# Performance work log

Hardware: AMD Instinct MI355X
Metric: run time of the kernel (lower is better)

The kernel has to match this reference:

```python
import jax, jax.numpy as jnp
import numpy as np

B = 32768
Z_DIM = 64
X_DIM = 256
HIDDEN = 512
T = 8            # num_transforms
NBINS = 8
TAIL = 25.0
MULT = 3 * NBINS - 1   # widths + heights + interior derivatives = 23
MIN_W = 1e-3
MIN_H = 1e-3
MIN_D = 1e-3


def _masks():
    # MADE degrees (nflows, random_mask=False)
    d_in = np.arange(1, Z_DIM + 1)                      # input degrees 1..D
    h = np.arange(HIDDEN) % (Z_DIM - 1) + 1             # hidden degrees
    o = np.arange(Z_DIM * MULT) // MULT + 1             # output degrees, MULT contiguous per feature
    m1 = (h[:, None] >= d_in[None, :]).astype(np.float32)   # [H, D]
    m2 = (h[:, None] >= h[None, :]).astype(np.float32)      # [H, H]
    m3 = (o[:, None] > h[None, :]).astype(np.float32)       # [D*MULT, H] strict for output layer
    return jnp.asarray(m1), jnp.asarray(m2), jnp.asarray(m3)


def _rq_spline_fwd(z, uw, uh, ud):
    """Unconstrained rational-quadratic spline with linear tails (forward).
    z: [B, D]; uw/uh: [B, D, NBINS]; ud: [B, D, NBINS-1].
    Returns (outputs [B,D], logabsdet [B,D])."""
    const = np.log(np.exp(1.0 - MIN_D) - 1.0)
    pad = jnp.full(ud.shape[:-1] + (1,), const, ud.dtype)
    ud = jnp.concatenate([pad, ud, pad], axis=-1)       # [B, D, NBINS+1]

    widths = jax.nn.softmax(uw, axis=-1)
    widths = MIN_W + (1.0 - MIN_W * NBINS) * widths
    zero = jnp.zeros(widths.shape[:-1] + (1,), widths.dtype)
    cumw = jnp.concatenate([zero, jnp.cumsum(widths, axis=-1)], axis=-1)
    cumw = -TAIL + 2.0 * TAIL * cumw
    cumw = cumw.at[..., 0].set(-TAIL).at[..., -1].set(TAIL)
    widths = cumw[..., 1:] - cumw[..., :-1]

    derivs = MIN_D + jax.nn.softplus(ud)

    heights = jax.nn.softmax(uh, axis=-1)
    heights = MIN_H + (1.0 - MIN_H * NBINS) * heights
    cumh = jnp.concatenate([zero, jnp.cumsum(heights, axis=-1)], axis=-1)
    cumh = -TAIL + 2.0 * TAIL * cumh
    cumh = cumh.at[..., 0].set(-TAIL).at[..., -1].set(TAIL)
    heights = cumh[..., 1:] - cumh[..., :-1]

    delta = heights / widths

    z_in = jnp.clip(z, -TAIL, TAIL)
    edges = cumw.at[..., -1].add(1e-6)                  # nflows searchsorted eps
    idx = jnp.sum(z_in[..., None] >= edges, axis=-1) - 1
    idx = jnp.clip(idx, 0, NBINS - 1)

    g = lambda a: jnp.take_along_axis(a, idx[..., None], axis=-1)[..., 0]
    in_cw = g(cumw); in_w = g(widths)
    in_ch = g(cumh); in_h = g(heights)
    in_dl = g(delta)
    d0 = g(derivs); d1 = g(derivs[..., 1:])

    th = (z_in - in_cw) / in_w
    th1 = th * (1.0 - th)
    num = in_h * (in_dl * th * th + d0 * th1)
    den = in_dl + (d0 + d1 - 2.0 * in_dl) * th1
    out = in_ch + num / den
    dnum = in_dl ** 2 * (d1 * th * th + 2.0 * in_dl * th1 + d0 * (1.0 - th) ** 2)
    lad = jnp.log(dnum) - 2.0 * jnp.log(den)

    inside = (z >= -TAIL) & (z <= TAIL)
    return jnp.where(inside, out, z), jnp.where(inside, lad, 0.0)


def setup_inputs() -> dict:
    key = jax.random.key(0)
    ks = jax.random.split(key, 10)
    s = 0.05  # small init scale keeps spline params in a sane regime
    return {
        "z": jax.random.normal(ks[0], (B, Z_DIM), jnp.float32),
        "x": jax.random.normal(ks[1], (B, X_DIM), jnp.float32),
        "W1": jax.random.normal(ks[2], (T, HIDDEN, Z_DIM), jnp.float32) * s,
        "b1": jax.random.normal(ks[3], (T, HIDDEN), jnp.float32) * s,
        "Wc": jax.random.normal(ks[4], (T, HIDDEN, X_DIM), jnp.float32) * s,
        "bc": jax.random.normal(ks[5], (T, HIDDEN), jnp.float32) * s,
        "W2": jax.random.normal(ks[6], (T, HIDDEN, HIDDEN), jnp.float32) * s,
        "b2": jax.random.normal(ks[7], (T, HIDDEN), jnp.float32) * s,
        "W3": jax.random.normal(ks[8], (T, Z_DIM * MULT, HIDDEN), jnp.float32) * s,
        "b3": jax.random.normal(ks[9], (T, Z_DIM * MULT), jnp.float32) * s,
    }


def reference(z, x, W1, b1, Wc, bc, W2, b2, W3, b3):
    """log q(z|x) of the composed MADE-RQ-spline flow, shape [B]."""
    m1, m2, m3 = _masks()
    inv_sqrt_h = 1.0 / np.sqrt(HIDDEN)
    cur = z
    total_lad = jnp.zeros(z.shape[0], z.dtype)
    for t in range(T):
        # MADE: masked initial layer + context layer, one masked feedforward block (linear->relu), masked output layer
        h = cur @ (W1[t] * m1).T + b1[t] + x @ Wc[t].T + bc[t]
        h = jax.nn.relu(h @ (W2[t] * m2).T + b2[t])
        p = (h @ (W3[t] * m3).T + b3[t]).reshape(-1, Z_DIM, MULT)
        uw = p[..., :NBINS] * inv_sqrt_h
        uh = p[..., NBINS:2 * NBINS] * inv_sqrt_h
        ud = p[..., 2 * NBINS:]
        cur, lad = _rq_spline_fwd(cur, uw, uh, ud)
        total_lad = total_lad + lad.sum(axis=-1)
    log_base = -0.5 * jnp.sum(cur ** 2, axis=-1) - 0.5 * Z_DIM * np.log(2.0 * np.pi)
    return log_base + total_lad
```

## Files before the change

kernel.cpp:

```cpp
#include <hip/hip_runtime.h>
#include <cstdint>
#include <cstddef>

#define B_ROWS 32768
#define ZD 64
#define XD 256
#define HID 512
#define T_STEPS 8
#define MULT 23
#define MPAD 24
#define NOUT 1472
#define NPAD 1536
#define K1 320
#define PSTRIDE 200

typedef float f32x4 __attribute__((ext_vector_type(4)));
typedef short s16x8 __attribute__((ext_vector_type(8)));

__device__ __forceinline__ unsigned short f2bf(float f) {
  unsigned int u = __float_as_uint(f);
  u = (u + 0x7FFFu + ((u >> 16) & 1u)) >> 16;
  return (unsigned short)u;
}
__device__ __forceinline__ float bf2f(unsigned short s) {
  return __uint_as_float(((unsigned int)s) << 16);
}

__device__ __forceinline__ int permP(int n) {
  return (n < 72) ? (n / 9) + 63 * (n % 9)
                  : ((n - 72) >> 3) + 8 + 63 * ((n - 72) & 7);
}
__device__ __forceinline__ int degP(int n) {
  return (n < 72) ? (n / 9) + 1 : ((n - 72) >> 3) + 9;
}


__global__ void prep_weights(const float* __restrict__ W1, const float* __restrict__ Wc,
                             const float* __restrict__ W2, const float* __restrict__ W3,
                             const float* __restrict__ b1, const float* __restrict__ bc,
                             const float* __restrict__ b2, const float* __restrict__ b3,
                             unsigned short* __restrict__ w1c, unsigned short* __restrict__ w2c,
                             unsigned short* __restrict__ w3c,
                             float* __restrict__ ob1, float* __restrict__ ob2,
                             float* __restrict__ ob3) {
  const int S1 = T_STEPS * HID * K1;
  const int S2 = S1 + T_STEPS * HID * HID;
  const int S3 = S2 + T_STEPS * NPAD * HID;
  const int S4 = S3 + T_STEPS * HID;
  const int S5 = S4 + T_STEPS * HID;
  const int S6 = S5 + T_STEPS * NPAD;
  int i = blockIdx.x * 256 + threadIdx.x;
  if (i < S1) {
    int t = i / (HID * K1);
    int r = i - t * (HID * K1);
    int n = r / K1;
    int k = r - n * K1;
    int on = permP(n);
    float v;
    if (k < ZD) v = ((on % 63) >= k) ? W1[((size_t)t * HID + on) * ZD + k] : 0.0f;
    else        v = Wc[((size_t)t * HID + on) * XD + (k - ZD)];
    w1c[i] = f2bf(v);
  } else if (i < S2) {
    int j = i - S1;
    int t = j / (HID * HID);
    int r = j - t * (HID * HID);
    int n = r / HID;
    int k = r - n * HID;
    float v = 0.0f;
    if (degP(n) >= degP(k))
      v = W2[((size_t)t * HID + permP(n)) * HID + permP(k)];
    w2c[j] = f2bf(v);
  } else if (i < S3) {
    int j = i - S2;
    int t = j / (NPAD * HID);
    int r = j - t * (NPAD * HID);
    int n = r / HID;
    int k = r - n * HID;
    int d = n / MPAD;
    int jj = n - d * MPAD;
    float v = 0.0f;
    if (jj < MULT && d >= degP(k))
      v = W3[((size_t)t * NOUT + d * MULT + jj) * HID + permP(k)];
    w3c[j] = f2bf(v);
  } else if (i < S4) {
    int j = i - S3;
    int t = j / HID, n = j - t * HID;
    int on = permP(n);
    ob1[j] = b1[(size_t)t * HID + on] + bc[(size_t)t * HID + on];
  } else if (i < S5) {
    int j = i - S4;
    int t = j / HID, n = j - t * HID;
    ob2[j] = b2[(size_t)t * HID + permP(n)];
  } else if (i < S6) {
    int j = i - S5;
    int t = j / NPAD;
    int n = j - t * NPAD;
    int d = n / MPAD;
    int jj = n - d * MPAD;
    ob3[j] = (jj < MULT) ? b3[(size_t)t * NOUT + d * MULT + jj] : 0.0f;
  }
}

__global__ void prep_data(const float* __restrict__ x, const float* __restrict__ z,
                          unsigned short* __restrict__ A1,
                          float* __restrict__ curf, float* __restrict__ out) {
  const int SX = B_ROWS * XD;
  int i = blockIdx.x * 256 + threadIdx.x;
  if (i < SX) {
    int b = i >> 8;
    int j = i & 255;
    A1[(size_t)b * K1 + ZD + j] = f2bf(x[i]);
  } else {
    int j = i - SX;
    if (j < B_ROWS * ZD) {
      int b = j >> 6;
      int d = j & 63;
      float zv = z[j];
      A1[(size_t)b * K1 + d] = f2bf(zv);
      curf[j] = zv;
      if (d == 0) out[b] = -58.81206612509905f;
    }
  }
}


#define ASYNC16(gp, lp) __builtin_amdgcn_global_load_lds( \
    (__attribute__((address_space(1))) unsigned int*)(gp), \
    (__attribute__((address_space(3))) unsigned int*)(lp), 16, 0, 0)

#define WAITV(n) asm volatile("s_waitcnt vmcnt(" #n ")" ::: "memory")


__global__ __launch_bounds__(256, 3) void gemm_bias(
    const unsigned short* __restrict__ A,
    const unsigned short* __restrict__ Bw,
    const float* __restrict__ bias,
    unsigned short* __restrict__ C,
    int M, int N, int K, int relu, int tri)
{
  __shared__ alignas(16) unsigned short lS[3][8192];

  const int tid  = threadIdx.x;
  const int lane = tid & 63;
  const int wave = tid >> 6;

  const int lin = blockIdx.y * 4 + blockIdx.x;
  const int xcd = lin & 7;
  const int loc = lin >> 3;
  const int m0 = (xcd * 32 + (loc >> 2)) * 128;
  const int n0 = (loc & 3) * 128;
  const int Keff = tri ? min(K, 192 + n0) : K;
  const int nIter = Keff >> 5;

  const int wm = (wave >> 1) * 64;
  const int wn = (wave & 1) * 64;

  const int f    = tid * 16;
  const int row0 = f >> 6;
  const int colb = f & 63;

  char* gA0 = (char*)A  + ((size_t)(m0 + row0) * K) * 2 + colb;
  char* gA1 = gA0 + (size_t)64 * K * 2;
  char* gB0 = (char*)Bw + ((size_t)(n0 + row0) * K) * 2 + colb;
  char* gB1 = gB0 + (size_t)64 * K * 2;

  f32x4 acc[4][4];
#pragma unroll
  for (int i = 0; i < 4; i++)
#pragma unroll
    for (int j = 0; j < 4; j++) acc[i][j] = (f32x4){0.f, 0.f, 0.f, 0.f};

  const int fr = lane & 15;
  const int fk = (lane >> 4) * 8;

#define STAGEB(sp) do { \
    unsigned short* s_ = (sp) + wave * 512; \
    ASYNC16(gA0, s_); \
    ASYNC16(gA1, s_ + 2048); \
    ASYNC16(gB0, s_ + 4096); \
    ASYNC16(gB1, s_ + 6144); \
    gA0 += 64; gA1 += 64; gB0 += 64; gB1 += 64; \
  } while (0)

  STAGEB(lS[0]);
  STAGEB(lS[1]);

  for (int k = 0; k < nIter; ++k) {
    __builtin_amdgcn_sched_barrier(0);
    if (k + 2 < nIter) STAGEB(lS[0] + ((k + 2) % 3) * 8192);
    const int nv = nIter - 1 - k;
    if (nv >= 2)      WAITV(8);
    else if (nv == 1) WAITV(4);
    else              WAITV(0);
    __builtin_amdgcn_s_barrier();
    __builtin_amdgcn_sched_barrier(0);

    const unsigned short* cs = lS[0] + (k % 3) * 8192;
    s16x8 a[4], b[4];
#pragma unroll
    for (int i = 0; i < 4; i++)
      a[i] = *(const s16x8*)(cs + (wm + i * 16 + fr) * 32 + fk);
#pragma unroll
    for (int j = 0; j < 4; j++)
      b[j] = *(const s16x8*)(cs + 4096 + (wn + j * 16 + fr) * 32 + fk);

#pragma unroll
    for (int i = 0; i < 4; i++)
#pragma unroll
      for (int j = 0; j < 4; j++)
        acc[i][j] = __builtin_amdgcn_mfma_f32_16x16x32_bf16(a[i], b[j], acc[i][j], 0, 0, 0);

    __builtin_amdgcn_sched_barrier(0);
    __builtin_amdgcn_s_barrier();
  }
#undef STAGEB

#pragma unroll
  for (int j = 0; j < 4; j++) {
    const int col = n0 + wn + j * 16 + fr;
    const float bv = bias[col];
#pragma unroll
    for (int i = 0; i < 4; i++) {
      const int rbase = m0 + wm + i * 16 + (lane >> 4) * 4;
#pragma unroll
      for (int r = 0; r < 4; r++) {
        float v = acc[i][j][r] + bv;
        if (relu) v = fmaxf(v, 0.0f);
        C[(size_t)(rbase + r) * N + col] = f2bf(v);
      }
    }
  }
}


__device__ __forceinline__ void rq_spline(const unsigned short* __restrict__ pp,
                                          float zv, float& zn, float& lad) {
  const float TAILC = 25.0f;
  const float MIN_WC = 0.001f;
  const float MIN_DC = 0.001f;
  const float SCALE2 = 0.06376007120095582f;
  const float LN2 = 0.6931471805599453f;

  s16x8 vw = *(const s16x8*)(pp);
  s16x8 vh = *(const s16x8*)(pp + 8);
  s16x8 vd = *(const s16x8*)(pp + 16);

  bool inside = (zv >= -TAILC) && (zv <= TAILC);
  float z_in = fminf(fmaxf(zv, -TAILC), TAILC);

  float ew[8], eh[8], sw = 0.f, sh = 0.f;
#pragma unroll
  for (int i = 0; i < 8; i++) {
    ew[i] = exp2f(bf2f((unsigned short)vw[i]) * SCALE2); sw += ew[i];
  }
#pragma unroll
  for (int i = 0; i < 8; i++) {
    eh[i] = exp2f(bf2f((unsigned short)vh[i]) * SCALE2); sh += eh[i];
  }
  float iw = (1.0f - 8.0f * MIN_WC) / sw;
  float ih = (1.0f - 8.0f * MIN_WC) / sh;

  float cumw[9], cumh[9];
  cumw[0] = -TAILC; cumh[0] = -TAILC;
  float cw = 0.f, ch = 0.f;
#pragma unroll
  for (int i = 0; i < 8; i++) {
    cw += MIN_WC + ew[i] * iw;
    ch += MIN_WC + eh[i] * ih;
    cumw[i + 1] = fmaf(2.0f * TAILC, cw, -TAILC);
    cumh[i + 1] = fmaf(2.0f * TAILC, ch, -TAILC);
  }
  cumw[8] = TAILC; cumh[8] = TAILC;

  int idx = 0;
#pragma unroll
  for (int i = 1; i < 8; i++) idx += (z_in >= cumw[i]) ? 1 : 0;

  float in_cw = 0.f, cw1 = 1.f, in_ch = 0.f, ch1 = 1.f, u0 = 0.f, u1 = 0.f;
#pragma unroll
  for (int i = 0; i < 8; i++) {
    if (i == idx) {
      in_cw = cumw[i]; cw1 = cumw[i + 1];
      in_ch = cumh[i]; ch1 = cumh[i + 1];
      u0 = (i > 0) ? bf2f((unsigned short)vd[i - 1]) : 0.0f;
      u1 = (i < 7) ? bf2f((unsigned short)vd[i]) : 0.0f;
    }
  }
  float dd0 = (idx == 0) ? 1.0f
            : MIN_DC + fmaxf(u0, 0.f) + __logf(1.0f + __expf(-fabsf(u0)));
  float dd1 = (idx == 7) ? 1.0f
            : MIN_DC + fmaxf(u1, 0.f) + __logf(1.0f + __expf(-fabsf(u1)));
  float in_w = cw1 - in_cw;
  float in_h = ch1 - in_ch;

  float delta = in_h / in_w;
  float th  = (z_in - in_cw) / in_w;
  float th1 = th * (1.0f - th);
  float th2 = th * th;
  float num = in_h * (delta * th2 + dd0 * th1);
  float den = delta + (dd0 + dd1 - 2.0f * delta) * th1;
  float outz = in_ch + num / den;
  float omt = 1.0f - th;
  float dnum = delta * delta * (dd1 * th2 + 2.0f * delta * th1 + dd0 * omt * omt);
  float l = LN2 * (__log2f(dnum) - 2.0f * __log2f(den));

  zn  = inside ? outz : zv;
  lad = inside ? l : 0.0f;
}


__global__ __launch_bounds__(256, 2) void gemm3_spline(
    const unsigned short* __restrict__ A,
    const unsigned short* __restrict__ Bw,
    const float* __restrict__ bias,
    float* __restrict__ curf,
    unsigned short* __restrict__ A1,
    float* __restrict__ out,
    int last)
{
  __shared__ alignas(16) union {
    unsigned short stage[3][10240];
    unsigned short p[128 * PSTRIDE];
  } sm;

  const int tid  = threadIdx.x;
  const int lane = tid & 63;
  const int wave = tid >> 6;

  const int lin = blockIdx.y * 8 + blockIdx.x;
  const int xcd = lin & 7;
  const int loc = lin >> 3;
  const int m0 = (xcd * 32 + (loc >> 3)) * 128;
  const int bn = loc & 7;
  const int n0 = bn * 192;
  const int nIter = 2 * (bn + 1);

  const int wm = (wave >> 1) * 64;
  const int wn = (wave & 1) * 96;
  const int fr = lane & 15;
  const int fk = (lane >> 4) * 8;

  const int srow = tid & 127;
  const int sb = m0 + srow;
  const int dl0 = (tid >> 7) * 4;
  const int d0 = bn * 8 + dl0;
  float4 cz = *(const float4*)(curf + (size_t)sb * ZD + d0);
  float bv[6];
#pragma unroll
  for (int j = 0; j < 6; j++) bv[j] = bias[n0 + wn + j * 16 + fr];

  const int f    = tid * 16;
  const int row0 = f >> 6;
  const int colb = f & 63;
  const int K = HID;

  char* gA0 = (char*)A  + ((size_t)(m0 + row0) * K) * 2 + colb;
  char* gA1 = gA0 + (size_t)64 * K * 2;
  char* gB0 = (char*)Bw + ((size_t)(n0 + row0) * K) * 2 + colb;
  char* gB1 = gB0 + (size_t)64 * K * 2;
  char* gB2 = gB1 + (size_t)64 * K * 2;

  f32x4 acc[4][6];
#pragma unroll
  for (int i = 0; i < 4; i++)
#pragma unroll
    for (int j = 0; j < 6; j++) acc[i][j] = (f32x4){0.f, 0.f, 0.f, 0.f};

#define STAGE3(sp) do { \
    unsigned short* s_ = (sp) + wave * 512; \
    ASYNC16(gA0, s_); \
    ASYNC16(gA1, s_ + 2048); \
    ASYNC16(gB0, s_ + 4096); \
    ASYNC16(gB1, s_ + 6144); \
    ASYNC16(gB2, s_ + 8192); \
    gA0 += 64; gA1 += 64; gB0 += 64; gB1 += 64; gB2 += 64; \
  } while (0)

  STAGE3(sm.stage[0]);
  STAGE3(sm.stage[1]);

  for (int k = 0; k < nIter; ++k) {
    __builtin_amdgcn_sched_barrier(0);
    if (k + 2 < nIter) STAGE3(sm.stage[0] + ((k + 2) % 3) * 10240);
    const int nv = nIter - 1 - k;
    if (nv >= 2)      WAITV(10);
    else if (nv == 1) WAITV(5);
    else              WAITV(0);
    __builtin_amdgcn_s_barrier();
    __builtin_amdgcn_sched_barrier(0);

    const unsigned short* cs = sm.stage[0] + (k % 3) * 10240;
    s16x8 a[4], b[6];
#pragma unroll
    for (int i = 0; i < 4; i++)
      a[i] = *(const s16x8*)(cs + (wm + i * 16 + fr) * 32 + fk);
#pragma unroll
    for (int j = 0; j < 6; j++)
      b[j] = *(const s16x8*)(cs + 4096 + (wn + j * 16 + fr) * 32 + fk);

#pragma unroll
    for (int i = 0; i < 4; i++)
#pragma unroll
      for (int j = 0; j < 6; j++)
        acc[i][j] = __builtin_amdgcn_mfma_f32_16x16x32_bf16(a[i], b[j], acc[i][j], 0, 0, 0);

    __builtin_amdgcn_sched_barrier(0);
    __builtin_amdgcn_s_barrier();
  }
#undef STAGE3

#pragma unroll
  for (int j = 0; j < 6; j++) {
    const int col = wn + j * 16 + fr;
#pragma unroll
    for (int i = 0; i < 4; i++) {
      const int rbase = wm + i * 16 + (lane >> 4) * 4;
#pragma unroll
      for (int r = 0; r < 4; r++)
        sm.p[(rbase + r) * PSTRIDE + col] = f2bf(acc[i][j][r] + bv[j]);
    }
  }
  __syncthreads();

  const unsigned short* pp = sm.p + srow * PSTRIDE + dl0 * MPAD;
  float zn0, zn1, zn2, zn3, l0, l1, l2, l3;
  rq_spline(pp,            cz.x, zn0, l0);
  rq_spline(pp + MPAD,     cz.y, zn1, l1);
  rq_spline(pp + 2 * MPAD, cz.z, zn2, l2);
  rq_spline(pp + 3 * MPAD, cz.w, zn3, l3);

  *(float4*)(curf + (size_t)sb * ZD + d0) = make_float4(zn0, zn1, zn2, zn3);
  union { unsigned int u[2]; unsigned short s[4]; } pk;
  pk.s[0] = f2bf(zn0); pk.s[1] = f2bf(zn1); pk.s[2] = f2bf(zn2); pk.s[3] = f2bf(zn3);
  *(uint2*)(A1 + (size_t)sb * K1 + d0) = make_uint2(pk.u[0], pk.u[1]);

  float contrib = l0 + l1 + l2 + l3;
  if (last)
    contrib -= 0.5f * (zn0 * zn0 + zn1 * zn1 + zn2 * zn2 + zn3 * zn3);
  atomicAdd(&out[sb], contrib);
}


extern "C" void kernel_launch(void* const* d_in, const int* in_sizes, int n_in,
                              void* d_out, int out_size, void* d_ws, size_t ws_size,
                              hipStream_t stream)
{
  const float* z  = (const float*)d_in[0];
  const float* x  = (const float*)d_in[1];
  const float* W1 = (const float*)d_in[2];
  const float* b1 = (const float*)d_in[3];
  const float* Wc = (const float*)d_in[4];
  const float* bc = (const float*)d_in[5];
  const float* W2 = (const float*)d_in[6];
  const float* b2 = (const float*)d_in[7];
  const float* W3 = (const float*)d_in[8];
  const float* b3 = (const float*)d_in[9];
  float* out = (float*)d_out;
  char* ws = (char*)d_ws;

  size_t oA1 = 0;
  size_t oH1 = oA1 + (size_t)B_ROWS * K1 * 2;
  size_t oH2 = oH1 + (size_t)B_ROWS * HID * 2;
  size_t oCU = oH2 + (size_t)B_ROWS * HID * 2;
  size_t oW1 = oCU + (size_t)B_ROWS * ZD * 4;
  size_t oW2 = oW1 + (size_t)T_STEPS * HID * K1 * 2;
  size_t oW3 = oW2 + (size_t)T_STEPS * HID * HID * 2;
  size_t oB1 = oW3 + (size_t)T_STEPS * NPAD * HID * 2;
  size_t oB2 = oB1 + (size_t)T_STEPS * HID * 4;
  size_t oB3 = oB2 + (size_t)T_STEPS * HID * 4;

  unsigned short* A1  = (unsigned short*)(ws + oA1);
  unsigned short* h1  = (unsigned short*)(ws + oH1);
  unsigned short* h2  = (unsigned short*)(ws + oH2);
  float* curf = (float*)(ws + oCU);
  unsigned short* w1c = (unsigned short*)(ws + oW1);
  unsigned short* w2c = (unsigned short*)(ws + oW2);
  unsigned short* w3c = (unsigned short*)(ws + oW3);
  float* b1c = (float*)(ws + oB1);
  float* b2p = (float*)(ws + oB2);
  float* b3c = (float*)(ws + oB3);

  const int prepw_total = T_STEPS * (HID * K1 + HID * HID + NPAD * HID + 2 * HID + NPAD);
  prep_weights<<<(prepw_total + 255) / 256, 256, 0, stream>>>(
      W1, Wc, W2, W3, b1, bc, b2, b3, w1c, w2c, w3c, b1c, b2p, b3c);
  const int prepd_total = B_ROWS * (XD + ZD);
  prep_data<<<(prepd_total + 255) / 256, 256, 0, stream>>>(x, z, A1, curf, out);

  for (int t = 0; t < T_STEPS; ++t) {
    gemm_bias<<<dim3(4, B_ROWS / 128), 256, 0, stream>>>(
        A1, w1c + (size_t)t * HID * K1, b1c + (size_t)t * HID, h1,
        B_ROWS, HID, K1, 0, 0);
    gemm_bias<<<dim3(4, B_ROWS / 128), 256, 0, stream>>>(
        h1, w2c + (size_t)t * HID * HID, b2p + (size_t)t * HID, h2,
        B_ROWS, HID, HID, 1, 1);
    gemm3_spline<<<dim3(8, B_ROWS / 128), 256, 0, stream>>>(
        h2, w3c + (size_t)t * NPAD * HID, b3c + (size_t)t * NPAD,
        curf, A1, out, (t == T_STEPS - 1) ? 1 : 0);
  }
}
```

Before: 1.045 ms.

## Load GEMM3 operands directly from global into registers, dropping LDS staging

The output-layer GEMM in the fused spline kernel no longer stages A and W tiles through a triple-buffered LDS pipeline with async copies and barriers. Each wave now reads its MFMA fragments straight from global memory into registers, double-buffered across 32-wide K steps. This removes the LDS traffic and block barriers but loses the cross-wave sharing of tiles, so global/L2 traffic rises and the loads are less coalesced (16-byte chunks per row with a stride of 1 KB).

```diff
diff --git a/kernel.cpp b/kernel.cpp
--- a/kernel.cpp
+++ b/kernel.cpp
@@ -318,10 +318,7 @@
     float* __restrict__ out,
     int last)
 {
-  __shared__ alignas(16) union {
-    unsigned short stage[3][10240];
-    unsigned short p[128 * PSTRIDE];
-  } sm;
+  __shared__ alignas(16) unsigned short p[128 * PSTRIDE];
 
   const int tid  = threadIdx.x;
   const int lane = tid & 63;
@@ -333,7 +330,7 @@
   const int m0 = (xcd * 32 + (loc >> 3)) * 128;
   const int bn = loc & 7;
   const int n0 = bn * 192;
-  const int nIter = 2 * (bn + 1);
+  const int Keff = 64 * (bn + 1);
 
   const int wm = (wave >> 1) * 64;
   const int wn = (wave & 1) * 96;
@@ -349,16 +346,8 @@
 #pragma unroll
   for (int j = 0; j < 6; j++) bv[j] = bias[n0 + wn + j * 16 + fr];
 
-  const int f    = tid * 16;
-  const int row0 = f >> 6;
-  const int colb = f & 63;
-  const int K = HID;
-
-  char* gA0 = (char*)A  + ((size_t)(m0 + row0) * K) * 2 + colb;
-  char* gA1 = gA0 + (size_t)64 * K * 2;
-  char* gB0 = (char*)Bw + ((size_t)(n0 + row0) * K) * 2 + colb;
-  char* gB1 = gB0 + (size_t)64 * K * 2;
-  char* gB2 = gB1 + (size_t)64 * K * 2;
+  const unsigned short* pa = A  + (((size_t)(m0 + wm + fr)) << 9) + fk;
+  const unsigned short* pb = Bw + (((size_t)(n0 + wn + fr)) << 9) + fk;
 
   f32x4 acc[4][6];
 #pragma unroll
@@ -366,48 +355,37 @@
 #pragma unroll
     for (int j = 0; j < 6; j++) acc[i][j] = (f32x4){0.f, 0.f, 0.f, 0.f};
 
-#define STAGE3(sp) do { \
-    unsigned short* s_ = (sp) + wave * 512; \
-    ASYNC16(gA0, s_); \
-    ASYNC16(gA1, s_ + 2048); \
-    ASYNC16(gB0, s_ + 4096); \
-    ASYNC16(gB1, s_ + 6144); \
-    ASYNC16(gB2, s_ + 8192); \
-    gA0 += 64; gA1 += 64; gB0 += 64; gB1 += 64; gB2 += 64; \
-  } while (0)
-
-  STAGE3(sm.stage[0]);
-  STAGE3(sm.stage[1]);
-
-  for (int k = 0; k < nIter; ++k) {
-    __builtin_amdgcn_sched_barrier(0);
-    if (k + 2 < nIter) STAGE3(sm.stage[0] + ((k + 2) % 3) * 10240);
-    const int nv = nIter - 1 - k;
-    if (nv >= 2)      WAITV(10);
-    else if (nv == 1) WAITV(5);
-    else              WAITV(0);
-    __builtin_amdgcn_s_barrier();
-    __builtin_amdgcn_sched_barrier(0);
-
-    const unsigned short* cs = sm.stage[0] + (k % 3) * 10240;
-    s16x8 a[4], b[6];
+  s16x8 a0[4], a1[4], b0[6], b1[6];
+#pragma unroll
+  for (int i = 0; i < 4; i++) a0[i] = *(const s16x8*)(pa + i * 8192);
+#pragma unroll
+  for (int j = 0; j < 6; j++) b0[j] = *(const s16x8*)(pb + j * 8192);
+
+  for (int k0 = 0; k0 < Keff; k0 += 64) {
+#pragma unroll
+    for (int i = 0; i < 4; i++) a1[i] = *(const s16x8*)(pa + i * 8192 + k0 + 32);
+#pragma unroll
+    for (int j = 0; j < 6; j++) b1[j] = *(const s16x8*)(pb + j * 8192 + k0 + 32);
+
 #pragma unroll
     for (int i = 0; i < 4; i++)
-      a[i] = *(const s16x8*)(cs + (wm + i * 16 + fr) * 32 + fk);
-#pragma unroll
-    for (int j = 0; j < 6; j++)
-      b[j] = *(const s16x8*)(cs + 4096 + (wn + j * 16 + fr) * 32 + fk);
+#pragma unroll
+      for (int j = 0; j < 6; j++)
+        acc[i][j] = __builtin_amdgcn_mfma_f32_16x16x32_bf16(a0[i], b0[j], acc[i][j], 0, 0, 0);
+
+    if (k0 + 64 < Keff) {
+#pragma unroll
+      for (int i = 0; i < 4; i++) a0[i] = *(const s16x8*)(pa + i * 8192 + k0 + 64);
+#pragma unroll
+      for (int j = 0; j < 6; j++) b0[j] = *(const s16x8*)(pb + j * 8192 + k0 + 64);
+    }
 
 #pragma unroll
     for (int i = 0; i < 4; i++)
 #pragma unroll
       for (int j = 0; j < 6; j++)
-        acc[i][j] = __builtin_amdgcn_mfma_f32_16x16x32_bf16(a[i], b[j], acc[i][j], 0, 0, 0);
-
-    __builtin_amdgcn_sched_barrier(0);
-    __builtin_amdgcn_s_barrier();
-  }
-#undef STAGE3
+        acc[i][j] = __builtin_amdgcn_mfma_f32_16x16x32_bf16(a1[i], b1[j], acc[i][j], 0, 0, 0);
+  }
 
 #pragma unroll
   for (int j = 0; j < 6; j++) {
@@ -417,12 +395,12 @@
       const int rbase = wm + i * 16 + (lane >> 4) * 4;
 #pragma unroll
       for (int r = 0; r < 4; r++)
-        sm.p[(rbase + r) * PSTRIDE + col] = f2bf(acc[i][j][r] + bv[j]);
+        p[(rbase + r) * PSTRIDE + col] = f2bf(acc[i][j][r] + bv[j]);
     }
   }
   __syncthreads();
 
-  const unsigned short* pp = sm.p + srow * PSTRIDE + dl0 * MPAD;
+  const unsigned short* pp = p + srow * PSTRIDE + dl0 * MPAD;
   float zn0, zn1, zn2, zn3, l0, l1, l2, l3;
   rq_spline(pp,            cz.x, zn0, l0);
   rq_spline(pp + MPAD,     cz.y, zn1, l1);
```

Result: slower. 1.581 ms (+51.3%).
